# Kernel optimization log

Hardware: AMD Instinct MI355X
Metric: run time of the kernel (lower is better)

## Reference

```python
import jax, jax.numpy as jnp
import numpy as np
from jax import lax

B, T, N_INPUT = 64, 2048, 257
HIDDEN = 32
N_OUTPUT = 10


def setup_inputs() -> dict:
    key = jax.random.key(0)
    ks = jax.random.split(key, 7)
    return {
        "specs": jax.random.normal(ks[0], (B, T, N_INPUT), dtype=jnp.float32),
        "W_ih": jax.random.normal(ks[1], (4 * HIDDEN, N_INPUT), dtype=jnp.float32) * 0.05,
        "W_hh": jax.random.normal(ks[2], (4 * HIDDEN, HIDDEN), dtype=jnp.float32) * 0.05,
        "b_ih": jax.random.normal(ks[3], (4 * HIDDEN,), dtype=jnp.float32) * 0.05,
        "b_hh": jax.random.normal(ks[4], (4 * HIDDEN,), dtype=jnp.float32) * 0.05,
        "W_out": jax.random.normal(ks[5], (N_OUTPUT, HIDDEN), dtype=jnp.float32) * 0.05,
        "b_out": jax.random.normal(ks[6], (N_OUTPUT,), dtype=jnp.float32) * 0.05,
    }


def reference(specs, W_ih, W_hh, b_ih, b_hh, W_out, b_out):
    # specs: [B, T, n_input]. PyTorch LSTMCell, gate order (i, f, g, o).
    b, t, _ = specs.shape
    h0 = jnp.zeros((b, HIDDEN), dtype=specs.dtype)
    c0 = jnp.zeros((b, HIDDEN), dtype=specs.dtype)
    # Precompute input projection for all timesteps in one GEMM: [B, T, 4H]
    x_proj = jnp.einsum("bti,gi->btg", specs, W_ih) + b_ih + b_hh
    x_proj = jnp.swapaxes(x_proj, 0, 1)  # [T, B, 4H] for scan

    def step(carry, xg):
        h, c = carry
        gates = xg + h @ W_hh.T  # [B, 4H]
        i, f, g, o = jnp.split(gates, 4, axis=-1)
        i = jax.nn.sigmoid(i)
        f = jax.nn.sigmoid(f)
        g = jnp.tanh(g)
        o = jax.nn.sigmoid(o)
        c = f * c + i * g
        h = o * jnp.tanh(c)
        return (h, c), None

    (hn, _), _ = lax.scan(step, (h0, c0), x_proj)
    logits = jax.nn.relu(hn) @ W_out.T + b_out  # [B, n_output]
    return jax.nn.log_softmax(logits, axis=1)
```

## Files before the change

kernel.cpp:

```cpp
#include <hip/hip_runtime.h>

#define B_SZ 64
#define T_LEN 2048
#define NIN 257
#define HID 32
#define G4 128
#define NOUT 10

#define TBT 128
#define PAD 34
#define CH 8
#define NSCAN 64
#define NGEMMP 1024
#define NTILE 1024
#define TPB 16

#define SC_SIG  -1.44269504f
#define SC_TANH -2.88539008f

typedef int v2i __attribute__((ext_vector_type(2)));
typedef unsigned long long u64;

#define DOT2(acc, w, hpk) \
  asm("v_dot2_f32_f16 %0, %1, %2, %0" : "+v"(acc) : "v"(w), "s"(hpk))

#define PKF16(dst, a, b) \
  asm("v_cvt_pkrtz_f16_f32 %0, %1, %2" : "=v"(dst) : "v"(a), "v"(b))

__device__ __forceinline__ void gemm_tile(
    const float* __restrict__ A, const float* __restrict__ W,
    const float* __restrict__ b_ih, const float* __restrict__ b_hh,
    float* __restrict__ C, int bt0, float* sA, float* sB)
{
  const int tid = threadIdx.x;
  const int gt = tid & 15;
  const int btt = tid >> 4;
  float acc[8][8];
#pragma unroll
  for (int i = 0; i < 8; ++i)
#pragma unroll
    for (int j = 0; j < 8; ++j) acc[i][j] = 0.f;

  for (int kc = 0; kc < 8; ++kc) {
    const int k0 = kc * 32;
    __syncthreads();
#pragma unroll
    for (int i = 0; i < 16; ++i) {
      int s = i * 256 + tid;
      int r = s >> 5, cc = s & 31;
      sA[r * PAD + cc] = A[(size_t)(bt0 + r) * NIN + k0 + cc];
      sB[r * PAD + cc] = W[(size_t)r * NIN + k0 + cc];
    }
    __syncthreads();
#pragma unroll
    for (int k2 = 0; k2 < 16; ++k2) {
      float2 a2[8], b2[8];
#pragma unroll
      for (int i = 0; i < 8; ++i)
        a2[i] = *(const float2*)&sA[(btt + 16 * i) * PAD + 2 * k2];
#pragma unroll
      for (int j = 0; j < 8; ++j)
        b2[j] = *(const float2*)&sB[(gt + 16 * j) * PAD + 2 * k2];
#pragma unroll
      for (int i = 0; i < 8; ++i)
#pragma unroll
        for (int j = 0; j < 8; ++j) {
          acc[i][j] = fmaf(a2[i].x, b2[j].x, acc[i][j]);
          acc[i][j] = fmaf(a2[i].y, b2[j].y, acc[i][j]);
        }
    }
  }
  {
    float a[8], bb[8];
#pragma unroll
    for (int i = 0; i < 8; ++i) a[i] = A[(size_t)(bt0 + btt + 16 * i) * NIN + 256];
#pragma unroll
    for (int j = 0; j < 8; ++j) bb[j] = W[(size_t)(gt + 16 * j) * NIN + 256];
#pragma unroll
    for (int i = 0; i < 8; ++i)
#pragma unroll
      for (int j = 0; j < 8; ++j) acc[i][j] += a[i] * bb[j];
  }
  float bias[8], sc[8];
  int off[8];
#pragma unroll
  for (int j = 0; j < 8; ++j) {
    const int col = gt + 16 * j;
    bias[j] = b_ih[col] + b_hh[col];
    sc[j] = ((col >> 5) == 2) ? SC_TANH : SC_SIG;
    off[j] = ((col & 63) << 1) + (col >> 6);
  }
#pragma unroll
  for (int i = 0; i < 8; ++i) {
    size_t row = (size_t)(bt0 + btt + 16 * i) * G4;
#pragma unroll
    for (int j = 0; j < 8; ++j) C[row + off[j]] = (acc[i][j] + bias[j]) * sc[j];
  }
}

__global__ __launch_bounds__(256) void fused(
    const float* __restrict__ A,
    const float* __restrict__ W,
    const float* __restrict__ b_ih,
    const float* __restrict__ b_hh,
    const float* __restrict__ W_hh,
    const float* __restrict__ W_out,
    const float* __restrict__ b_out,
    float* __restrict__ out,
    float* __restrict__ xproj,
    int* __restrict__ flags,
    int nowait)
{
  __shared__ float sA[TBT * PAD];
  __shared__ float sB[G4 * PAD];
  const int bid = blockIdx.x;

  if (bid >= NSCAN) {
    const int p = bid - NSCAN;
    for (int idx = p; idx < NTILE; idx += NGEMMP) {
      const int ti = idx >> 6, bb = idx & 63;
      const int bt0 = bb * T_LEN + ti * TBT;
      gemm_tile(A, W, b_ih, b_hh, xproj, bt0, sA, sB);
      __threadfence();
      __syncthreads();
      if (threadIdx.x == 0)
        __hip_atomic_store(&flags[idx], 1, __ATOMIC_RELEASE, __HIP_MEMORY_SCOPE_AGENT);
    }
    return;
  }

  if (threadIdx.x >= 64) return;
  __builtin_amdgcn_s_setprio(3);
  const int b = bid;
  const int l = threadIdx.x;

  const float wsB = (l < HID) ? SC_TANH : SC_SIG;
  unsigned wA[16], wB[16];
#pragma unroll
  for (int j = 0; j < 16; j += 2) {
    float4 v0 = *(const float4*)&W_hh[l * HID + 2 * j];
    PKF16(wA[j],     v0.x * SC_SIG, v0.y * SC_SIG);
    PKF16(wA[j + 1], v0.z * SC_SIG, v0.w * SC_SIG);
    float4 v1 = *(const float4*)&W_hh[(l + 64) * HID + 2 * j];
    PKF16(wB[j],     v1.x * wsB, v1.y * wsB);
    PKF16(wB[j + 1], v1.z * wsB, v1.w * wsB);
  }

  float c = 0.f, h = 0.f;
  unsigned hp[16];
#pragma unroll
  for (int k = 0; k < 16; ++k) hp[k] = 0u;

  const float2* xb2 = (const float2*)(xproj + (size_t)b * T_LEN * G4);

  auto step = [&](float xa, float xg) {
    float aA0 = xa,  aA1 = 0.f, aA2 = 0.f, aA3 = 0.f;
    float aB0 = xg,  aB1 = 0.f, aB2 = 0.f, aB3 = 0.f;
#pragma unroll
    for (int j = 0; j < 4; ++j) {
      DOT2(aA0, wA[j],      hp[j]);
      DOT2(aA1, wA[4 + j],  hp[4 + j]);
      DOT2(aA2, wA[8 + j],  hp[8 + j]);
      DOT2(aA3, wA[12 + j], hp[12 + j]);
      DOT2(aB0, wB[j],      hp[j]);
      DOT2(aB1, wB[4 + j],  hp[4 + j]);
      DOT2(aB2, wB[8 + j],  hp[8 + j]);
      DOT2(aB3, wB[12 + j], hp[12 + j]);
    }
    float accA = (aA0 + aA1) + (aA2 + aA3);
    float accB = (aB0 + aB1) + (aB2 + aB3);
    float actA = __builtin_amdgcn_rcpf(1.f + __builtin_amdgcn_exp2f(accA));
    float sB2  = __builtin_amdgcn_rcpf(1.f + __builtin_amdgcn_exp2f(accB));
    float m1 = actA * (2.f * SC_TANH);
    float sh = sB2 - 0.5f;
    float prod = m1 * sh;
    v2i sw = __builtin_amdgcn_permlane32_swap(0, __float_as_int(prod), false, false);
    float pr = __int_as_float(sw[0]);
    c = fmaf(actA, c, pr);
    float t  = __builtin_amdgcn_rcpf(1.f + __builtin_amdgcn_exp2f(c));
    float s2 = sB2 + sB2;
    h = fmaf(s2, t, -sB2);
    int hn = __builtin_amdgcn_mov_dpp(__float_as_int(h), 0xF5, 0xF, 0xF, false);
    int pk;
    PKF16(pk, h, __int_as_float(hn));
#pragma unroll
    for (int k = 0; k < 16; ++k)
      hp[k] = (unsigned)__builtin_amdgcn_readlane(pk, 32 + 2 * k);
  };

  float2 X0[CH], X1[CH];
#define LOADC2(X, P) do { _Pragma("unroll") \
  for (int i = 0; i < CH; ++i) X[i] = (P)[i * 64]; } while (0)
#define STEPS(X) do { _Pragma("unroll") \
  for (int i = 0; i < CH; ++i) step(X[i].x, X[i].y); } while (0)

  for (int ti = 0; ti < TPB; ++ti) {
    if (!nowait) {
      while (__hip_atomic_load(&flags[ti * 64 + b], __ATOMIC_ACQUIRE,
                               __HIP_MEMORY_SCOPE_AGENT) == 0)
        __builtin_amdgcn_s_sleep(2);
    }
    const float2* xt = xb2 + (size_t)ti * TBT * 64 + l;
    LOADC2(X0, xt);
#pragma unroll 1
    for (int ch = 0; ch < TBT / CH; ch += 2) {
      const float2* s1 = xt + (size_t)(ch + 1) * CH * 64;
      LOADC2(X1, s1);
      STEPS(X0);
      if (ch + 2 < TBT / CH) {
        const float2* s2 = xt + (size_t)(ch + 2) * CH * 64;
        LOADC2(X0, s2);
      }
      STEPS(X1);
    }
  }

  float hf[HID];
#pragma unroll
  for (int k = 0; k < HID; ++k)
    hf[k] = __int_as_float(__builtin_amdgcn_readlane(__float_as_int(h), 32 + k));
  float logit = 0.f;
  if (l < NOUT) {
    logit = b_out[l];
#pragma unroll
    for (int j = 0; j < HID; ++j) logit += fmaxf(hf[j], 0.f) * W_out[l * HID + j];
  }
  float m = -1e30f;
#pragma unroll
  for (int n = 0; n < NOUT; ++n) m = fmaxf(m, __shfl(logit, n));
  float s = 0.f;
#pragma unroll
  for (int n = 0; n < NOUT; ++n)
    s += __builtin_amdgcn_exp2f(1.44269504089f * (__shfl(logit, n) - m));
  if (l < NOUT)
    out[b * NOUT + l] = logit - m - 0.69314718056f * __builtin_amdgcn_logf(s);
}

__global__ __launch_bounds__(256) void xproj_gemm(
    const float* __restrict__ A, const float* __restrict__ W,
    const float* __restrict__ b_ih, const float* __restrict__ b_hh,
    float* __restrict__ C)
{
  __shared__ float sA[TBT * PAD];
  __shared__ float sB[G4 * PAD];
  const int idx = blockIdx.x;
  const int ti = idx >> 6, bb = idx & 63;
  gemm_tile(A, W, b_ih, b_hh, C, bb * T_LEN + ti * TBT, sA, sB);
}

extern "C" void kernel_launch(void* const* d_in, const int* in_sizes, int n_in,
                              void* d_out, int out_size, void* d_ws, size_t ws_size,
                              hipStream_t stream) {
  const float* specs = (const float*)d_in[0];
  const float* W_ih  = (const float*)d_in[1];
  const float* W_hh  = (const float*)d_in[2];
  const float* b_ih  = (const float*)d_in[3];
  const float* b_hh  = (const float*)d_in[4];
  const float* W_out = (const float*)d_in[5];
  const float* b_out = (const float*)d_in[6];
  float* outp  = (float*)d_out;
  float* xproj = (float*)d_ws;
  const size_t xbytes = (size_t)B_SZ * T_LEN * G4 * 4;

  if (ws_size >= xbytes + NTILE * sizeof(int)) {
    int* flags = (int*)((char*)d_ws + xbytes);
    (void)hipMemsetAsync(flags, 0, NTILE * sizeof(int), stream);
    fused<<<NSCAN + NGEMMP, 256, 0, stream>>>(specs, W_ih, b_ih, b_hh, W_hh,
                                              W_out, b_out, outp, xproj, flags, 0);
  } else {
    xproj_gemm<<<NTILE, 256, 0, stream>>>(specs, W_ih, b_ih, b_hh, xproj);
    fused<<<NSCAN, 256, 0, stream>>>(specs, W_ih, b_ih, b_hh, W_hh,
                                     W_out, b_out, outp, xproj, (int*)xproj , 1);
  }
}
```

Before: 525.1 us.

## Interleave two independent batch recurrences per scan wavefront

Each scan wavefront now carries two batch rows and alternates their LSTM steps, so the dependent dot2, exp, rcp and lane-exchange chain of one row can overlap with the other's. This halves the number of scan blocks from 64 to 32 and is meant to hide the per-step latency of the serial recurrence. In exchange, each wavefront runs twice as many total instructions serially, uses more registers, and must wait on two GEMM tile flags per time block.

```diff
diff --git a/kernel.cpp b/kernel.cpp
--- a/kernel.cpp
+++ b/kernel.cpp
@@ -10,7 +10,7 @@
 #define TBT 128
 #define PAD 34
 #define CH 8
-#define NSCAN 64
+#define NSCANB 32
 #define NGEMMP 1024
 #define NTILE 1024
 #define TPB 16
@@ -115,8 +115,8 @@
   __shared__ float sB[G4 * PAD];
   const int bid = blockIdx.x;
 
-  if (bid >= NSCAN) {
-    const int p = bid - NSCAN;
+  if (bid >= NSCANB) {
+    const int p = bid - NSCANB;
     for (int idx = p; idx < NTILE; idx += NGEMMP) {
       const int ti = idx >> 6, bb = idx & 63;
       const int bt0 = bb * T_LEN + ti * TBT;
@@ -131,7 +131,7 @@
 
   if (threadIdx.x >= 64) return;
   __builtin_amdgcn_s_setprio(3);
-  const int b = bid;
+  const int w = bid;
   const int l = threadIdx.x;
 
   const float wsB = (l < HID) ? SC_TANH : SC_SIG;
@@ -146,14 +146,15 @@
     PKF16(wB[j + 1], v1.z * wsB, v1.w * wsB);
   }
 
-  float c = 0.f, h = 0.f;
-  unsigned hp[16];
-#pragma unroll
-  for (int k = 0; k < 16; ++k) hp[k] = 0u;
-
-  const float2* xb2 = (const float2*)(xproj + (size_t)b * T_LEN * G4);
-
-  auto step = [&](float xa, float xg) {
+  float c0 = 0.f, h0 = 0.f, c1 = 0.f, h1 = 0.f;
+  unsigned hp0[16], hp1[16];
+#pragma unroll
+  for (int k = 0; k < 16; ++k) { hp0[k] = 0u; hp1[k] = 0u; }
+
+  const float2* xbA = (const float2*)(xproj + (size_t)(2 * w)     * T_LEN * G4);
+  const float2* xbB = (const float2*)(xproj + (size_t)(2 * w + 1) * T_LEN * G4);
+
+  auto step = [&](float xa, float xg, float& c, float& h, unsigned* hp) {
     float aA0 = xa,  aA1 = 0.f, aA2 = 0.f, aA3 = 0.f;
     float aB0 = xg,  aB1 = 0.f, aB2 = 0.f, aB3 = 0.f;
 #pragma unroll
@@ -188,52 +189,74 @@
       hp[k] = (unsigned)__builtin_amdgcn_readlane(pk, 32 + 2 * k);
   };
 
-  float2 X0[CH], X1[CH];
+  float2 XA0[CH], XA1[CH], XB0[CH], XB1[CH];
 #define LOADC2(X, P) do { _Pragma("unroll") \
   for (int i = 0; i < CH; ++i) X[i] = (P)[i * 64]; } while (0)
-#define STEPS(X) do { _Pragma("unroll") \
-  for (int i = 0; i < CH; ++i) step(X[i].x, X[i].y); } while (0)
+#define STEPS2(XA, XB) do { _Pragma("unroll") \
+  for (int i = 0; i < CH; ++i) { \
+    step(XA[i].x, XA[i].y, c0, h0, hp0); \
+    step(XB[i].x, XB[i].y, c1, h1, hp1); \
+  } } while (0)
 
   for (int ti = 0; ti < TPB; ++ti) {
     if (!nowait) {
-      while (__hip_atomic_load(&flags[ti * 64 + b], __ATOMIC_ACQUIRE,
+      while (__hip_atomic_load(&flags[ti * 64 + 2 * w], __ATOMIC_ACQUIRE,
                                __HIP_MEMORY_SCOPE_AGENT) == 0)
         __builtin_amdgcn_s_sleep(2);
-    }
-    const float2* xt = xb2 + (size_t)ti * TBT * 64 + l;
-    LOADC2(X0, xt);
+      while (__hip_atomic_load(&flags[ti * 64 + 2 * w + 1], __ATOMIC_ACQUIRE,
+                               __HIP_MEMORY_SCOPE_AGENT) == 0)
+        __builtin_amdgcn_s_sleep(2);
+    }
+    const float2* pA = xbA + (size_t)ti * TBT * 64 + l;
+    const float2* pB = xbB + (size_t)ti * TBT * 64 + l;
+    LOADC2(XA0, pA);
+    LOADC2(XB0, pB);
 #pragma unroll 1
     for (int ch = 0; ch < TBT / CH; ch += 2) {
-      const float2* s1 = xt + (size_t)(ch + 1) * CH * 64;
-      LOADC2(X1, s1);
-      STEPS(X0);
+      LOADC2(XA1, pA + (size_t)(ch + 1) * CH * 64);
+      LOADC2(XB1, pB + (size_t)(ch + 1) * CH * 64);
+      STEPS2(XA0, XB0);
       if (ch + 2 < TBT / CH) {
-        const float2* s2 = xt + (size_t)(ch + 2) * CH * 64;
-        LOADC2(X0, s2);
+        LOADC2(XA0, pA + (size_t)(ch + 2) * CH * 64);
+        LOADC2(XB0, pB + (size_t)(ch + 2) * CH * 64);
       }
-      STEPS(X1);
-    }
-  }
-
-  float hf[HID];
-#pragma unroll
-  for (int k = 0; k < HID; ++k)
-    hf[k] = __int_as_float(__builtin_amdgcn_readlane(__float_as_int(h), 32 + k));
-  float logit = 0.f;
+      STEPS2(XA1, XB1);
+    }
+  }
+
+  float hf0[HID], hf1[HID];
+#pragma unroll
+  for (int k = 0; k < HID; ++k) {
+    hf0[k] = __int_as_float(__builtin_amdgcn_readlane(__float_as_int(h0), 32 + k));
+    hf1[k] = __int_as_float(__builtin_amdgcn_readlane(__float_as_int(h1), 32 + k));
+  }
+  float lg0 = 0.f, lg1 = 0.f;
   if (l < NOUT) {
-    logit = b_out[l];
-#pragma unroll
-    for (int j = 0; j < HID; ++j) logit += fmaxf(hf[j], 0.f) * W_out[l * HID + j];
-  }
-  float m = -1e30f;
-#pragma unroll
-  for (int n = 0; n < NOUT; ++n) m = fmaxf(m, __shfl(logit, n));
-  float s = 0.f;
-#pragma unroll
-  for (int n = 0; n < NOUT; ++n)
-    s += __builtin_amdgcn_exp2f(1.44269504089f * (__shfl(logit, n) - m));
-  if (l < NOUT)
-    out[b * NOUT + l] = logit - m - 0.69314718056f * __builtin_amdgcn_logf(s);
+    lg0 = b_out[l];
+    lg1 = b_out[l];
+#pragma unroll
+    for (int j = 0; j < HID; ++j) {
+      float wv = W_out[l * HID + j];
+      lg0 += fmaxf(hf0[j], 0.f) * wv;
+      lg1 += fmaxf(hf1[j], 0.f) * wv;
+    }
+  }
+  float m0 = -1e30f, m1 = -1e30f;
+#pragma unroll
+  for (int n = 0; n < NOUT; ++n) {
+    m0 = fmaxf(m0, __shfl(lg0, n));
+    m1 = fmaxf(m1, __shfl(lg1, n));
+  }
+  float s0 = 0.f, s1 = 0.f;
+#pragma unroll
+  for (int n = 0; n < NOUT; ++n) {
+    s0 += __builtin_amdgcn_exp2f(1.44269504089f * (__shfl(lg0, n) - m0));
+    s1 += __builtin_amdgcn_exp2f(1.44269504089f * (__shfl(lg1, n) - m1));
+  }
+  if (l < NOUT) {
+    out[(2 * w) * NOUT + l]     = lg0 - m0 - 0.69314718056f * __builtin_amdgcn_logf(s0);
+    out[(2 * w + 1) * NOUT + l] = lg1 - m1 - 0.69314718056f * __builtin_amdgcn_logf(s1);
+  }
 }
 
 __global__ __launch_bounds__(256) void xproj_gemm(
@@ -265,11 +288,11 @@
   if (ws_size >= xbytes + NTILE * sizeof(int)) {
     int* flags = (int*)((char*)d_ws + xbytes);
     (void)hipMemsetAsync(flags, 0, NTILE * sizeof(int), stream);
-    fused<<<NSCAN + NGEMMP, 256, 0, stream>>>(specs, W_ih, b_ih, b_hh, W_hh,
-                                              W_out, b_out, outp, xproj, flags, 0);
+    fused<<<NSCANB + NGEMMP, 256, 0, stream>>>(specs, W_ih, b_ih, b_hh, W_hh,
+                                               W_out, b_out, outp, xproj, flags, 0);
   } else {
     xproj_gemm<<<NTILE, 256, 0, stream>>>(specs, W_ih, b_ih, b_hh, xproj);
-    fused<<<NSCAN, 256, 0, stream>>>(specs, W_ih, b_ih, b_hh, W_hh,
-                                     W_out, b_out, outp, xproj, (int*)xproj , 1);
-  }
-}
+    fused<<<NSCANB, 256, 0, stream>>>(specs, W_ih, b_ih, b_hh, W_hh,
+                                      W_out, b_out, outp, xproj, (int*)xproj , 1);
+  }
+}
```

Measured after the change: 817.7 us. +55.7%, slower.

## Run LSTM recurrence with MFMA across 16 batches per block

Applied to the files above, without the earlier changes.

The recurrence now uses 4 scan blocks of 512 threads, each processing 16 batch rows together. The h·W_hh product is done per step with a 16x16x32 f16 MFMA, and h is exchanged through double-buffered LDS with a block barrier per step, replacing the per-batch single-wave dot2/readlane scheme. The GEMM writes xproj in a new interleaved layout that matches the MFMA accumulator fragment, and its tile is remapped to 512 threads. The intent is to cut per-step instruction count and scan-wave count, at the price of a __syncthreads on every timestep and each scan block now waiting on 16 tiles' flags.

```diff
diff --git a/kernel.cpp b/kernel.cpp
--- a/kernel.cpp
+++ b/kernel.cpp
@@ -9,8 +9,7 @@
 
 #define TBT 128
 #define PAD 34
-#define CH 8
-#define NSCAN 64
+#define NSCANB 4
 #define NGEMMP 1024
 #define NTILE 1024
 #define TPB 16
@@ -18,26 +17,29 @@
 #define SC_SIG  -1.44269504f
 #define SC_TANH -2.88539008f
 
-typedef int v2i __attribute__((ext_vector_type(2)));
-typedef unsigned long long u64;
-
-#define DOT2(acc, w, hpk) \
-  asm("v_dot2_f32_f16 %0, %1, %2, %0" : "+v"(acc) : "v"(w), "s"(hpk))
+typedef float f32x4v __attribute__((ext_vector_type(4)));
+typedef _Float16 f16x8v __attribute__((ext_vector_type(4 * 2)));
+typedef unsigned ux4v __attribute__((ext_vector_type(4)));
 
 #define PKF16(dst, a, b) \
   asm("v_cvt_pkrtz_f16_f32 %0, %1, %2" : "=v"(dst) : "v"(a), "v"(b))
+
+__device__ __forceinline__ float sig_e2(float x) {
+  return __builtin_amdgcn_rcpf(1.f + __builtin_amdgcn_exp2f(x));
+}
 
 __device__ __forceinline__ void gemm_tile(
     const float* __restrict__ A, const float* __restrict__ W,
     const float* __restrict__ b_ih, const float* __restrict__ b_hh,
-    float* __restrict__ C, int bt0, float* sA, float* sB)
+    float* __restrict__ C, int bb, int t0, float* sA, float* sB)
 {
   const int tid = threadIdx.x;
   const int gt = tid & 15;
-  const int btt = tid >> 4;
-  float acc[8][8];
-#pragma unroll
-  for (int i = 0; i < 8; ++i)
+  const int rw = tid >> 4;
+  const int bt0 = bb * T_LEN + t0;
+  float acc[4][8];
+#pragma unroll
+  for (int i = 0; i < 4; ++i)
 #pragma unroll
     for (int j = 0; j < 8; ++j) acc[i][j] = 0.f;
 
@@ -45,8 +47,8 @@
     const int k0 = kc * 32;
     __syncthreads();
 #pragma unroll
-    for (int i = 0; i < 16; ++i) {
-      int s = i * 256 + tid;
+    for (int it = 0; it < 8; ++it) {
+      int s = it * 512 + tid;
       int r = s >> 5, cc = s & 31;
       sA[r * PAD + cc] = A[(size_t)(bt0 + r) * NIN + k0 + cc];
       sB[r * PAD + cc] = W[(size_t)r * NIN + k0 + cc];
@@ -54,15 +56,15 @@
     __syncthreads();
 #pragma unroll
     for (int k2 = 0; k2 < 16; ++k2) {
-      float2 a2[8], b2[8];
-#pragma unroll
-      for (int i = 0; i < 8; ++i)
-        a2[i] = *(const float2*)&sA[(btt + 16 * i) * PAD + 2 * k2];
+      float2 a2[4], b2[8];
+#pragma unroll
+      for (int i = 0; i < 4; ++i)
+        a2[i] = *(const float2*)&sA[(rw + 32 * i) * PAD + 2 * k2];
 #pragma unroll
       for (int j = 0; j < 8; ++j)
         b2[j] = *(const float2*)&sB[(gt + 16 * j) * PAD + 2 * k2];
 #pragma unroll
-      for (int i = 0; i < 8; ++i)
+      for (int i = 0; i < 4; ++i)
 #pragma unroll
         for (int j = 0; j < 8; ++j) {
           acc[i][j] = fmaf(a2[i].x, b2[j].x, acc[i][j]);
@@ -71,34 +73,38 @@
     }
   }
   {
-    float a[8], bb[8];
-#pragma unroll
-    for (int i = 0; i < 8; ++i) a[i] = A[(size_t)(bt0 + btt + 16 * i) * NIN + 256];
-#pragma unroll
-    for (int j = 0; j < 8; ++j) bb[j] = W[(size_t)(gt + 16 * j) * NIN + 256];
-#pragma unroll
-    for (int i = 0; i < 8; ++i)
-#pragma unroll
-      for (int j = 0; j < 8; ++j) acc[i][j] += a[i] * bb[j];
+    float a[4], bb2[8];
+#pragma unroll
+    for (int i = 0; i < 4; ++i) a[i] = A[(size_t)(bt0 + rw + 32 * i) * NIN + 256];
+#pragma unroll
+    for (int j = 0; j < 8; ++j) bb2[j] = W[(size_t)(gt + 16 * j) * NIN + 256];
+#pragma unroll
+    for (int i = 0; i < 4; ++i)
+#pragma unroll
+      for (int j = 0; j < 8; ++j) acc[i][j] += a[i] * bb2[j];
   }
   float bias[8], sc[8];
-  int off[8];
 #pragma unroll
   for (int j = 0; j < 8; ++j) {
     const int col = gt + 16 * j;
     bias[j] = b_ih[col] + b_hh[col];
     sc[j] = ((col >> 5) == 2) ? SC_TANH : SC_SIG;
-    off[j] = ((col & 63) << 1) + (col >> 6);
-  }
-#pragma unroll
-  for (int i = 0; i < 8; ++i) {
-    size_t row = (size_t)(bt0 + btt + 16 * i) * G4;
-#pragma unroll
-    for (int j = 0; j < 8; ++j) C[row + off[j]] = (acc[i][j] + bias[j]) * sc[j];
-  }
-}
-
-__global__ __launch_bounds__(256) void fused(
+  }
+  const size_t gbase = (size_t)(bb >> 4) * T_LEN * 2048;
+  const int cc4 = (bb & 15) * 4;
+  const int me = (gt >> 2) * 256 + (gt & 3) * 64 + cc4;
+#pragma unroll
+  for (int i = 0; i < 4; ++i) {
+    const int t = t0 + rw + 32 * i;
+    float* p = C + gbase + (size_t)t * 2048 + me;
+    *(float4*)p = make_float4((acc[i][0] + bias[0]) * sc[0], (acc[i][2] + bias[2]) * sc[2],
+                              (acc[i][4] + bias[4]) * sc[4], (acc[i][6] + bias[6]) * sc[6]);
+    *(float4*)(p + 1024) = make_float4((acc[i][1] + bias[1]) * sc[1], (acc[i][3] + bias[3]) * sc[3],
+                                       (acc[i][5] + bias[5]) * sc[5], (acc[i][7] + bias[7]) * sc[7]);
+  }
+}
+
+__global__ __launch_bounds__(512) void fused(
     const float* __restrict__ A,
     const float* __restrict__ W,
     const float* __restrict__ b_ih,
@@ -113,130 +119,130 @@
 {
   __shared__ float sA[TBT * PAD];
   __shared__ float sB[G4 * PAD];
+  __shared__ _Float16 Hbuf[1024];
+  __shared__ float Hf[16][HID];
+  __shared__ float Lg[16][NOUT];
   const int bid = blockIdx.x;
-
-  if (bid >= NSCAN) {
-    const int p = bid - NSCAN;
+  const int tid = threadIdx.x;
+
+  if (bid >= NSCANB) {
+    const int p = bid - NSCANB;
     for (int idx = p; idx < NTILE; idx += NGEMMP) {
       const int ti = idx >> 6, bb = idx & 63;
-      const int bt0 = bb * T_LEN + ti * TBT;
-      gemm_tile(A, W, b_ih, b_hh, xproj, bt0, sA, sB);
+      gemm_tile(A, W, b_ih, b_hh, xproj, bb, ti * TBT, sA, sB);
       __threadfence();
       __syncthreads();
-      if (threadIdx.x == 0)
+      if (tid == 0)
         __hip_atomic_store(&flags[idx], 1, __ATOMIC_RELEASE, __HIP_MEMORY_SCOPE_AGENT);
     }
     return;
   }
 
-  if (threadIdx.x >= 64) return;
   __builtin_amdgcn_s_setprio(3);
-  const int b = bid;
-  const int l = threadIdx.x;
-
-  const float wsB = (l < HID) ? SC_TANH : SC_SIG;
-  unsigned wA[16], wB[16];
-#pragma unroll
-  for (int j = 0; j < 16; j += 2) {
-    float4 v0 = *(const float4*)&W_hh[l * HID + 2 * j];
-    PKF16(wA[j],     v0.x * SC_SIG, v0.y * SC_SIG);
-    PKF16(wA[j + 1], v0.z * SC_SIG, v0.w * SC_SIG);
-    float4 v1 = *(const float4*)&W_hh[(l + 64) * HID + 2 * j];
-    PKF16(wB[j],     v1.x * wsB, v1.y * wsB);
-    PKF16(wB[j + 1], v1.z * wsB, v1.w * wsB);
-  }
-
-  float c = 0.f, h = 0.f;
-  unsigned hp[16];
-#pragma unroll
-  for (int k = 0; k < 16; ++k) hp[k] = 0u;
-
-  const float2* xb2 = (const float2*)(xproj + (size_t)b * T_LEN * G4);
-
-  auto step = [&](float xa, float xg) {
-    float aA0 = xa,  aA1 = 0.f, aA2 = 0.f, aA3 = 0.f;
-    float aB0 = xg,  aB1 = 0.f, aB2 = 0.f, aB3 = 0.f;
-#pragma unroll
-    for (int j = 0; j < 4; ++j) {
-      DOT2(aA0, wA[j],      hp[j]);
-      DOT2(aA1, wA[4 + j],  hp[4 + j]);
-      DOT2(aA2, wA[8 + j],  hp[8 + j]);
-      DOT2(aA3, wA[12 + j], hp[12 + j]);
-      DOT2(aB0, wB[j],      hp[j]);
-      DOT2(aB1, wB[4 + j],  hp[4 + j]);
-      DOT2(aB2, wB[8 + j],  hp[8 + j]);
-      DOT2(aB3, wB[12 + j], hp[12 + j]);
-    }
-    float accA = (aA0 + aA1) + (aA2 + aA3);
-    float accB = (aB0 + aB1) + (aB2 + aB3);
-    float actA = __builtin_amdgcn_rcpf(1.f + __builtin_amdgcn_exp2f(accA));
-    float sB2  = __builtin_amdgcn_rcpf(1.f + __builtin_amdgcn_exp2f(accB));
-    float m1 = actA * (2.f * SC_TANH);
-    float sh = sB2 - 0.5f;
-    float prod = m1 * sh;
-    v2i sw = __builtin_amdgcn_permlane32_swap(0, __float_as_int(prod), false, false);
-    float pr = __int_as_float(sw[0]);
-    c = fmaf(actA, c, pr);
-    float t  = __builtin_amdgcn_rcpf(1.f + __builtin_amdgcn_exp2f(c));
-    float s2 = sB2 + sB2;
-    h = fmaf(s2, t, -sB2);
-    int hn = __builtin_amdgcn_mov_dpp(__float_as_int(h), 0xF5, 0xF, 0xF, false);
-    int pk;
-    PKF16(pk, h, __int_as_float(hn));
-#pragma unroll
-    for (int k = 0; k < 16; ++k)
-      hp[k] = (unsigned)__builtin_amdgcn_readlane(pk, 32 + 2 * k);
+  const int g  = bid;
+  const int mt = tid >> 6;
+  const int l  = tid & 63;
+  const int cB = l & 15;
+  const int qD = l >> 4;
+  const int hidO = 4 * mt + qD;
+
+  f16x8v afrag;
+  {
+    const int arow = l & 15;
+    const int ahid = 4 * mt + (arow >> 2);
+    const int agate = arow & 3;
+    const float asc = (agate == 2) ? SC_TANH : SC_SIG;
+    const float* wr = W_hh + (size_t)(agate * HID + ahid) * HID + (l >> 4) * 8;
+    float4 wv0 = *(const float4*)wr;
+    float4 wv1 = *(const float4*)(wr + 4);
+    unsigned u0, u1, u2, u3;
+    PKF16(u0, wv0.x * asc, wv0.y * asc);
+    PKF16(u1, wv0.z * asc, wv0.w * asc);
+    PKF16(u2, wv1.x * asc, wv1.y * asc);
+    PKF16(u3, wv1.z * asc, wv1.w * asc);
+    ux4v au = {u0, u1, u2, u3};
+    afrag = __builtin_bit_cast(f16x8v, au);
+  }
+
+  Hbuf[tid] = (_Float16)0.f;
+  __syncthreads();
+
+  const int rbase = cB * 32 + 8 * qD;
+  const int wbase = cB * 32 + hidO;
+  int bufo = 0;
+  float cst = 0.f, hcur = 0.f;
+
+  auto step = [&](f32x4v xc) {
+    ux4v bu = *(const ux4v*)&Hbuf[bufo + rbase];
+    f16x8v bf = __builtin_bit_cast(f16x8v, bu);
+    f32x4v d = __builtin_amdgcn_mfma_f32_16x16x32_f16(afrag, bf, xc, 0, 0, 0);
+    float i_ = sig_e2(d[0]);
+    float f_ = sig_e2(d[1]);
+    float sg = sig_e2(d[2]);
+    float o_ = sig_e2(d[3]);
+    float m1 = i_ * (2.f * SC_TANH);
+    float sh = sg - 0.5f;
+    cst = fmaf(f_, cst, m1 * sh);
+    float tt = sig_e2(cst);
+    hcur = fmaf(o_ + o_, tt, -o_);
+    Hbuf[(bufo ^ 512) + wbase] = (_Float16)hcur;
+    __syncthreads();
+    bufo ^= 512;
   };
 
-  float2 X0[CH], X1[CH];
-#define LOADC2(X, P) do { _Pragma("unroll") \
-  for (int i = 0; i < CH; ++i) X[i] = (P)[i * 64]; } while (0)
-#define STEPS(X) do { _Pragma("unroll") \
-  for (int i = 0; i < CH; ++i) step(X[i].x, X[i].y); } while (0)
+  const float* xbase = xproj + (size_t)g * T_LEN * 2048 +
+                       (size_t)mt * 256 + qD * 64 + cB * 4;
+#define LX(X, base, t4) do { \
+    (X)[0] = *(const f32x4v*)((base) + (size_t)((t4) + 0) * 2048); \
+    (X)[1] = *(const f32x4v*)((base) + (size_t)((t4) + 1) * 2048); \
+    (X)[2] = *(const f32x4v*)((base) + (size_t)((t4) + 2) * 2048); \
+    (X)[3] = *(const f32x4v*)((base) + (size_t)((t4) + 3) * 2048); \
+  } while (0)
 
   for (int ti = 0; ti < TPB; ++ti) {
     if (!nowait) {
-      while (__hip_atomic_load(&flags[ti * 64 + b], __ATOMIC_ACQUIRE,
+      const int fidx = ti * 64 + 16 * g + cB;
+      while (__hip_atomic_load(&flags[fidx], __ATOMIC_ACQUIRE,
                                __HIP_MEMORY_SCOPE_AGENT) == 0)
         __builtin_amdgcn_s_sleep(2);
     }
-    const float2* xt = xb2 + (size_t)ti * TBT * 64 + l;
-    LOADC2(X0, xt);
+    const float* xt = xbase + (size_t)ti * TBT * 2048;
+    f32x4v X0[4], X1[4];
+    LX(X0, xt, 0);
 #pragma unroll 1
-    for (int ch = 0; ch < TBT / CH; ch += 2) {
-      const float2* s1 = xt + (size_t)(ch + 1) * CH * 64;
-      LOADC2(X1, s1);
-      STEPS(X0);
-      if (ch + 2 < TBT / CH) {
-        const float2* s2 = xt + (size_t)(ch + 2) * CH * 64;
-        LOADC2(X0, s2);
-      }
-      STEPS(X1);
-    }
-  }
-
-  float hf[HID];
-#pragma unroll
-  for (int k = 0; k < HID; ++k)
-    hf[k] = __int_as_float(__builtin_amdgcn_readlane(__float_as_int(h), 32 + k));
-  float logit = 0.f;
-  if (l < NOUT) {
-    logit = b_out[l];
-#pragma unroll
-    for (int j = 0; j < HID; ++j) logit += fmaxf(hf[j], 0.f) * W_out[l * HID + j];
-  }
-  float m = -1e30f;
-#pragma unroll
-  for (int n = 0; n < NOUT; ++n) m = fmaxf(m, __shfl(logit, n));
-  float s = 0.f;
-#pragma unroll
-  for (int n = 0; n < NOUT; ++n)
-    s += __builtin_amdgcn_exp2f(1.44269504089f * (__shfl(logit, n) - m));
-  if (l < NOUT)
-    out[b * NOUT + l] = logit - m - 0.69314718056f * __builtin_amdgcn_logf(s);
-}
-
-__global__ __launch_bounds__(256) void xproj_gemm(
+    for (int u = 0; u < 16; ++u) {
+      LX(X1, xt, 8 * u + 4);
+      step(X0[0]); step(X0[1]); step(X0[2]); step(X0[3]);
+      if (u < 15) LX(X0, xt, 8 * u + 8);
+      step(X1[0]); step(X1[1]); step(X1[2]); step(X1[3]);
+    }
+  }
+
+  Hf[cB][hidO] = fmaxf(hcur, 0.f);
+  __syncthreads();
+  if (tid < 16 * NOUT) {
+    const int cb = tid / NOUT, n = tid - cb * NOUT;
+    float lg = b_out[n];
+#pragma unroll
+    for (int j = 0; j < HID; ++j) lg += Hf[cb][j] * W_out[n * HID + j];
+    Lg[cb][n] = lg;
+  }
+  __syncthreads();
+  if (tid < 16 * NOUT) {
+    const int cb = tid / NOUT, n = tid - cb * NOUT;
+    float mx = -1e30f;
+#pragma unroll
+    for (int k = 0; k < NOUT; ++k) mx = fmaxf(mx, Lg[cb][k]);
+    float ss = 0.f;
+#pragma unroll
+    for (int k = 0; k < NOUT; ++k)
+      ss += __builtin_amdgcn_exp2f(1.44269504089f * (Lg[cb][k] - mx));
+    out[(16 * g + cb) * NOUT + n] =
+        Lg[cb][n] - mx - 0.69314718056f * __builtin_amdgcn_logf(ss);
+  }
+}
+
+__global__ __launch_bounds__(512) void xproj_gemm(
     const float* __restrict__ A, const float* __restrict__ W,
     const float* __restrict__ b_ih, const float* __restrict__ b_hh,
     float* __restrict__ C)
@@ -245,7 +251,7 @@
   __shared__ float sB[G4 * PAD];
   const int idx = blockIdx.x;
   const int ti = idx >> 6, bb = idx & 63;
-  gemm_tile(A, W, b_ih, b_hh, C, bb * T_LEN + ti * TBT, sA, sB);
+  gemm_tile(A, W, b_ih, b_hh, C, bb, ti * TBT, sA, sB);
 }
 
 extern "C" void kernel_launch(void* const* d_in, const int* in_sizes, int n_in,
@@ -265,11 +271,11 @@
   if (ws_size >= xbytes + NTILE * sizeof(int)) {
     int* flags = (int*)((char*)d_ws + xbytes);
     (void)hipMemsetAsync(flags, 0, NTILE * sizeof(int), stream);
-    fused<<<NSCAN + NGEMMP, 256, 0, stream>>>(specs, W_ih, b_ih, b_hh, W_hh,
-                                              W_out, b_out, outp, xproj, flags, 0);
+    fused<<<NSCANB + NGEMMP, 512, 0, stream>>>(specs, W_ih, b_ih, b_hh, W_hh,
+                                               W_out, b_out, outp, xproj, flags, 0);
   } else {
-    xproj_gemm<<<NTILE, 256, 0, stream>>>(specs, W_ih, b_ih, b_hh, xproj);
-    fused<<<NSCAN, 256, 0, stream>>>(specs, W_ih, b_ih, b_hh, W_hh,
-                                     W_out, b_out, outp, xproj, (int*)xproj , 1);
-  }
-}
+    xproj_gemm<<<NTILE, 512, 0, stream>>>(specs, W_ih, b_ih, b_hh, xproj);
+    fused<<<NSCANB, 512, 0, stream>>>(specs, W_ih, b_ih, b_hh, W_hh,
+                                      W_out, b_out, outp, xproj, (int*)xproj , 1);
+  }
+}
```

Result: slower. 902.4 us (+71.9%).
